# Kernel tuning notes

Measured on AMD Instinct MI355X. Metric: run time of the kernel, lower is better.

The kernel has to match this reference:

```python
import jax, jax.numpy as jnp
import numpy as np

B, S, H, D = 2, 2048, 16, 64
HID = H * D
NEG_INF = -10000.0

def setup_inputs() -> dict:
    key = jax.random.key(0)
    ks = jax.random.split(key, 4)
    std = 0.02
    return {
        'x': jax.random.normal(ks[0], (B, S, HID), dtype=jnp.float32),
        'mask': jnp.ones((B, S), dtype=jnp.int32),
        'Wq': jax.random.normal(ks[1], (HID, HID), dtype=jnp.float32) * std,
        'bq': jnp.zeros((HID,), dtype=jnp.float32),
        'Wk': jax.random.normal(ks[2], (HID, HID), dtype=jnp.float32) * std,
        'bk': jnp.zeros((HID,), dtype=jnp.float32),
        'Wv': jax.random.normal(ks[3], (HID, HID), dtype=jnp.float32) * std,
        'bv': jnp.zeros((HID,), dtype=jnp.float32),
    }

def reference(x, mask, Wq, bq, Wk, bk, Wv, bv):
    b, s, _ = x.shape
    def split_heads(t):  # [b,s,HID] -> [b,H,s,D]
        return t.reshape(b, s, H, D).transpose(0, 2, 1, 3)
    q = split_heads(x @ Wq + bq)
    k = split_heads(x @ Wk + bk)
    v = split_heads(x @ Wv + bv)
    scores = jnp.einsum('bhqd,bhkd->bhqk', q, k) / jnp.sqrt(jnp.float32(D))
    # additive padding mask: [b,1,1,s] broadcast over query positions and heads
    adder = (1.0 - mask.astype(scores.dtype))[:, None, None, :] * NEG_INF
    probs = jax.nn.softmax(scores + adder, axis=-1)
    ctx = jnp.einsum('bhqk,bhkd->bhqd', probs, v)  # [b,H,s,D]
    return ctx.transpose(0, 2, 1, 3).reshape(b, s, HID)
```

## Files before the change

### kernel.cpp

```cpp
#include <hip/hip_runtime.h>
#include <cstddef>

constexpr int Bc = 2, Sc = 2048, Hc = 16, Dc = 64, HIDc = 1024;
#define NEG_INF -10000.0f
#define LOG2E 1.44269504088896340736f

typedef _Float16 half8  __attribute__((ext_vector_type(8)));
typedef _Float16 half4  __attribute__((ext_vector_type(4)));
typedef float   floatx4 __attribute__((ext_vector_type(4)));

__device__ __forceinline__ void gload_lds16(const void* g, void* l) {
    __builtin_amdgcn_global_load_lds(
        (const __attribute__((address_space(1))) unsigned int*)g,
        (__attribute__((address_space(3))) unsigned int*)l, 16, 0, 0);
}

__global__ __launch_bounds__(256) void cvt_x_kernel(const float* __restrict__ x,
                                                    _Float16* __restrict__ xh) {
    int i = (blockIdx.x * 256 + threadIdx.x) * 8;
    float4 a = *(const float4*)(x + i);
    float4 b = *(const float4*)(x + i + 4);
    half8 h;
    h[0] = (_Float16)a.x; h[1] = (_Float16)a.y; h[2] = (_Float16)a.z; h[3] = (_Float16)a.w;
    h[4] = (_Float16)b.x; h[5] = (_Float16)b.y; h[6] = (_Float16)b.z; h[7] = (_Float16)b.w;
    *(half8*)(xh + i) = h;
}

__global__ __launch_bounds__(256) void cvt_w_kernel(const float* __restrict__ Wq,
                                                    const float* __restrict__ Wk,
                                                    const float* __restrict__ Wv,
                                                    _Float16* __restrict__ Wt) {
    const float* W = (blockIdx.z == 0) ? Wq : (blockIdx.z == 1) ? Wk : Wv;
    _Float16* out = Wt + (size_t)blockIdx.z * HIDc * HIDc;
    __shared__ _Float16 T[64][65];
    const int t = threadIdx.x;
    const int kb = blockIdx.x * 64, nb = blockIdx.y * 64;
    const int r = t >> 2, c4 = (t & 3) * 16;
    #pragma unroll
    for (int i = 0; i < 16; i += 4) {
        float4 a = *(const float4*)(W + (size_t)(kb + r) * HIDc + nb + c4 + i);
        T[c4 + i + 0][r] = (_Float16)a.x;
        T[c4 + i + 1][r] = (_Float16)a.y;
        T[c4 + i + 2][r] = (_Float16)a.z;
        T[c4 + i + 3][r] = (_Float16)a.w;
    }
    __syncthreads();
    const int n = t >> 2, k4 = (t & 3) * 16;
    half8 o0, o1;
    #pragma unroll
    for (int j = 0; j < 8; ++j) { o0[j] = T[n][k4 + j]; o1[j] = T[n][k4 + 8 + j]; }
    *(half8*)(out + (size_t)(nb + n) * HIDc + kb + k4)     = o0;
    *(half8*)(out + (size_t)(nb + n) * HIDc + kb + k4 + 8) = o1;
}

__global__ __launch_bounds__(256, 3) void proj_kernel(
    const _Float16* __restrict__ xh, const _Float16* __restrict__ Wt,
    const float* __restrict__ bq, const float* __restrict__ bk, const float* __restrict__ bv,
    _Float16* __restrict__ qw, _Float16* __restrict__ kw, _Float16* __restrict__ vt)
{
    const int z = blockIdx.z;
    const _Float16* Wz = Wt + (size_t)z * HIDc * HIDc;
    const float* bias = (z == 0) ? bq : (z == 1) ? bk : bv;

    __shared__ __align__(16) _Float16 SM[2][2][128 * 32];

    const int t = threadIdx.x;
    const int lane = t & 63, w = t >> 6;
    const int quad = lane >> 4, l16 = lane & 15;
    const int m0 = blockIdx.y * 128, n0 = blockIdx.x * 128;
    const int wm = (w >> 1) * 64, wn = (w & 1) * 64;

    const int srl = lane >> 2;
    const int ssl = (lane & 3) ^ ((lane >> 3) & 3);

    floatx4 acc[4][4];
    #pragma unroll
    for (int mb = 0; mb < 4; ++mb)
        #pragma unroll
        for (int nb = 0; nb < 4; ++nb) acc[mb][nb] = floatx4{0.f, 0.f, 0.f, 0.f};

    auto stage = [&](int buf, int kt) {
        #pragma unroll
        for (int j = 0; j < 2; ++j) {
            const int rb = (w + 4 * j) * 16;
            gload_lds16(xh + (size_t)(m0 + rb + srl) * HIDc + kt + ssl * 8,
                        &SM[buf][0][rb * 32]);
            gload_lds16(Wz + (size_t)(n0 + rb + srl) * HIDc + kt + ssl * 8,
                        &SM[buf][1][rb * 32]);
        }
    };

    stage(0, 0);
    __syncthreads();

    const int sA = (quad ^ ((l16 >> 1) & 3)) * 8;

    #pragma unroll 2
    for (int it = 0; it < HIDc / 32; ++it) {
        const int cur = it & 1;
        const int kn = (it + 1 < HIDc / 32) ? (it + 1) * 32 : 0;
        stage(cur ^ 1, kn);

        half8 af[4], bf[4];
        #pragma unroll
        for (int mb = 0; mb < 4; ++mb)
            af[mb] = *(const half8*)(&SM[cur][0][(wm + mb * 16 + l16) * 32 + sA]);
        #pragma unroll
        for (int nb = 0; nb < 4; ++nb)
            bf[nb] = *(const half8*)(&SM[cur][1][(wn + nb * 16 + l16) * 32 + sA]);
        #pragma unroll
        for (int mb = 0; mb < 4; ++mb)
            #pragma unroll
            for (int nb = 0; nb < 4; ++nb)
                acc[mb][nb] = __builtin_amdgcn_mfma_f32_16x16x32_f16(
                    af[mb], bf[nb], acc[mb][nb], 0, 0, 0);
        __syncthreads();
    }

    if (z == 2) {
        _Float16* T = (_Float16*)SM;
        const int bI0 = m0 >> 11, m0s = m0 & (Sc - 1);
        #pragma unroll
        for (int p = 0; p < 2; ++p) {
            __syncthreads();
            if ((w & 1) == p) {
                #pragma unroll
                for (int nb = 0; nb < 4; ++nb) {
                    const int n = nb * 16 + l16;
                    const float bi = bias[n0 + p * 64 + n];
                    #pragma unroll
                    for (int mb = 0; mb < 4; ++mb) {
                        half4 h4;
                        #pragma unroll
                        for (int r = 0; r < 4; ++r)
                            h4[r] = (_Float16)(acc[mb][nb][r] + bi);
                        *(half4*)(T + n * 136 + wm + mb * 16 + quad * 4) = h4;
                    }
                }
            }
            __syncthreads();
            const int n = t >> 2;
            const int N = n0 + p * 64 + n, hh = N >> 6, d = N & 63;
            _Float16* vrow = vt + (((size_t)(bI0 * Hc + hh)) * Dc + d) * Sc + m0s;
            #pragma unroll
            for (int j = 0; j < 4; ++j) {
                const int c = (t & 3) * 32 + j * 8;
                *(uint4*)(vrow + c) = *(const uint4*)(T + n * 136 + c);
            }
        }
        return;
    }
    #pragma unroll
    for (int nb = 0; nb < 4; ++nb) {
        const int N = n0 + wn + nb * 16 + l16;
        const float bi = bias[N];
        const int h = N >> 6, d = N & 63;
        #pragma unroll
        for (int mb = 0; mb < 4; ++mb) {
            #pragma unroll
            for (int r = 0; r < 4; ++r) {
                const int M = m0 + wm + mb * 16 + quad * 4 + r;
                const int bI = M >> 11, s = M & (Sc - 1);
                const float v = acc[mb][nb][r] + bi;
                if (z == 0)
                    qw[(((size_t)(bI * Hc + h)) * Sc + s) * Dc + d] =
                        (_Float16)(v * (0.125f * LOG2E));
                else
                    kw[(((size_t)(bI * Hc + h)) * Sc + s) * Dc + d] = (_Float16)v;
            }
        }
    }
}

__global__ __launch_bounds__(256, 2) void attn_kernel(
    const _Float16* __restrict__ qw, const _Float16* __restrict__ kw,
    const _Float16* __restrict__ vt, const int* __restrict__ mask,
    float* __restrict__ out)
{
    __shared__ __align__(16) float adder[Sc];
    __shared__ __align__(16) _Float16 Ks[2][64][72];
    __shared__ __align__(16) _Float16 Vs[2][64][72];

    const int t = threadIdx.x;
    const int lane = t & 63, w = t >> 6;
    const int quad = lane >> 4, l16 = lane & 15;
    const int bh = blockIdx.y;
    const int bI = bh >> 4, h = bh & 15;

    const _Float16* Qp = qw + (size_t)bh * Sc * Dc;
    const _Float16* Kp = kw + (size_t)bh * Sc * Dc;
    const _Float16* Vp = vt + (size_t)bh * Dc * Sc;

    const int srow = t >> 3;
    const int scol = (t & 7) * 8;
    const int m7 = t & 7;
    const int vc0 = 32 * (m7 & 1) + 4 * (m7 >> 1);

    {
        const int4* mp = (const int4*)(mask + bI * Sc);
        #pragma unroll
        for (int i = 0; i < 2; ++i) {
            int4 m4 = mp[t * 2 + i];
            int base = (t * 2 + i) * 4;
            adder[base + 0] = (1.0f - (float)m4.x) * (NEG_INF * LOG2E);
            adder[base + 1] = (1.0f - (float)m4.y) * (NEG_INF * LOG2E);
            adder[base + 2] = (1.0f - (float)m4.z) * (NEG_INF * LOG2E);
            adder[base + 3] = (1.0f - (float)m4.w) * (NEG_INF * LOG2E);
        }
    }
    #pragma unroll
    for (int hf = 0; hf < 2; ++hf) {
        const int row = srow + 32 * hf;
        uint4 kv = *(const uint4*)(Kp + (size_t)row * Dc + scol);
        uint4 vv = *(const uint4*)(Vp + (size_t)row * Sc + scol);
        *(uint4*)(&Ks[0][row][scol]) = kv;
        *(uint2*)(&Vs[0][row][vc0])      = make_uint2(vv.x, vv.y);
        *(uint2*)(&Vs[0][row][vc0 + 16]) = make_uint2(vv.z, vv.w);
    }

    const int qrow = blockIdx.x * 128 + w * 32;
    half8 aq[2][2];
    #pragma unroll
    for (int s = 0; s < 2; ++s)
        #pragma unroll
        for (int hh = 0; hh < 2; ++hh)
            aq[s][hh] = *(const half8*)(Qp + (size_t)(qrow + 16 * s + l16) * Dc
                                        + hh * 32 + quad * 8);

    floatx4 o[2][4], osum[2];
    #pragma unroll
    for (int s = 0; s < 2; ++s) {
        osum[s] = floatx4{0.f, 0.f, 0.f, 0.f};
        #pragma unroll
        for (int db = 0; db < 4; ++db) o[s][db] = floatx4{0.f, 0.f, 0.f, 0.f};
    }
    const half4 ones4 = {(_Float16)1.f, (_Float16)1.f, (_Float16)1.f, (_Float16)1.f};

    __syncthreads();

    #pragma unroll 2
    for (int it = 0; it < Sc / 64; ++it) {
        const int cur = it & 1;
        const int kt = it * 64;
        const int ktn = (it + 1 < Sc / 64) ? kt + 64 : 0;
        uint4 kstg[2], vstg[2];
        #pragma unroll
        for (int hf = 0; hf < 2; ++hf) {
            const int row = srow + 32 * hf;
            kstg[hf] = *(const uint4*)(Kp + (size_t)(ktn + row) * Dc + scol);
            vstg[hf] = *(const uint4*)(Vp + (size_t)row * Sc + ktn + scol);
        }

        half8 kb[4][2];
        #pragma unroll
        for (int nb = 0; nb < 4; ++nb)
            #pragma unroll
            for (int hh = 0; hh < 2; ++hh)
                kb[nb][hh] = *(const half8*)(&Ks[cur][nb * 16 + l16][hh * 32 + quad * 8]);

        half4 vb[4][4];
        #pragma unroll
        for (int db = 0; db < 4; ++db)
            #pragma unroll
            for (int hf2 = 0; hf2 < 2; ++hf2) {
                const half8 v8 = *(const half8*)(&Vs[cur][db * 16 + l16][quad * 16 + hf2 * 8]);
                vb[hf2 * 2 + 0][db] = __builtin_shufflevector(v8, v8, 0, 1, 2, 3);
                vb[hf2 * 2 + 1][db] = __builtin_shufflevector(v8, v8, 4, 5, 6, 7);
            }

        floatx4 st[2][4];
        __builtin_amdgcn_s_setprio(1);
        #pragma unroll
        for (int nb = 0; nb < 4; ++nb) {
            const floatx4 adv = *(const floatx4*)(&adder[kt + nb * 16 + quad * 4]);
            #pragma unroll
            for (int s = 0; s < 2; ++s) {
                floatx4 x0 = __builtin_amdgcn_mfma_f32_16x16x32_f16(kb[nb][0], aq[s][0], adv, 0, 0, 0);
                st[s][nb]  = __builtin_amdgcn_mfma_f32_16x16x32_f16(kb[nb][1], aq[s][1], x0, 0, 0, 0);
            }
        }
        __builtin_amdgcn_s_setprio(0);

        half4 pa[2][4];
        #pragma unroll
        for (int s = 0; s < 2; ++s)
            #pragma unroll
            for (int nb = 0; nb < 4; ++nb)
                #pragma unroll
                for (int r = 0; r < 4; ++r)
                    pa[s][nb][r] = (_Float16)__builtin_amdgcn_exp2f(st[s][nb][r]);

        __builtin_amdgcn_s_setprio(1);
        #pragma unroll
        for (int s = 0; s < 2; ++s)
            #pragma unroll
            for (int nb = 0; nb < 4; ++nb) {
                osum[s] = __builtin_amdgcn_mfma_f32_16x16x16f16(pa[s][nb], ones4, osum[s], 0, 0, 0);
                #pragma unroll
                for (int db = 0; db < 4; ++db)
                    o[s][db] = __builtin_amdgcn_mfma_f32_16x16x16f16(
                        pa[s][nb], vb[nb][db], o[s][db], 0, 0, 0);
            }
        __builtin_amdgcn_s_setprio(0);

        #pragma unroll
        for (int hf = 0; hf < 2; ++hf) {
            const int row = srow + 32 * hf;
            *(uint4*)(&Ks[cur ^ 1][row][scol]) = kstg[hf];
            const uint4 vv = vstg[hf];
            *(uint2*)(&Vs[cur ^ 1][row][vc0])      = make_uint2(vv.x, vv.y);
            *(uint2*)(&Vs[cur ^ 1][row][vc0 + 16]) = make_uint2(vv.z, vv.w);
        }
        __syncthreads();
    }

    float* op = out + (size_t)bI * Sc * HIDc + h * Dc;
    #pragma unroll
    for (int s = 0; s < 2; ++s)
        #pragma unroll
        for (int r = 0; r < 4; ++r) {
            const float inv = __builtin_amdgcn_rcpf(osum[s][r]);
            const int q = qrow + 16 * s + quad * 4 + r;
            #pragma unroll
            for (int db = 0; db < 4; ++db)
                op[(size_t)q * HIDc + db * 16 + l16] = o[s][db][r] * inv;
        }
}

extern "C" void kernel_launch(void* const* d_in, const int* in_sizes, int n_in,
                              void* d_out, int out_size, void* d_ws, size_t ws_size,
                              hipStream_t stream) {
    const float* x    = (const float*)d_in[0];
    const int*   mask = (const int*)  d_in[1];
    const float* Wq   = (const float*)d_in[2];
    const float* bq   = (const float*)d_in[3];
    const float* Wk   = (const float*)d_in[4];
    const float* bk   = (const float*)d_in[5];
    const float* Wv   = (const float*)d_in[6];
    const float* bv   = (const float*)d_in[7];
    float* out = (float*)d_out;

    char* ws = (char*)d_ws;
    _Float16* xh = (_Float16*)(ws);
    _Float16* Wt = (_Float16*)(ws + (size_t)8  * 1024 * 1024);
    _Float16* qw = (_Float16*)(ws + (size_t)14 * 1024 * 1024);
    _Float16* kw = (_Float16*)(ws + (size_t)22 * 1024 * 1024);
    _Float16* vt = (_Float16*)(ws + (size_t)30 * 1024 * 1024);

    cvt_x_kernel<<<(Bc * Sc * HIDc) / (256 * 8), 256, 0, stream>>>(x, xh);
    cvt_w_kernel<<<dim3(HIDc / 64, HIDc / 64, 3), 256, 0, stream>>>(Wq, Wk, Wv, Wt);
    proj_kernel<<<dim3(HIDc / 128, (Bc * Sc) / 128, 3), 256, 0, stream>>>(
        xh, Wt, bq, bk, bv, qw, kw, vt);
    attn_kernel<<<dim3(Sc / 128, Bc * Hc), 256, 0, stream>>>(qw, kw, vt, mask, out);
}
```

Measured before the change: 168.5 us.

## Load V fragments directly from global and stage 128-key K tiles in LDS

V is no longer staged through shared memory. Each wave reads its V MFMA operands straight from global memory (the transposed V layout) as half4 loads. K tiles grow from 64 to 128 keys per iteration, and each iteration processes two 64-key halves, which halves the number of barriers and LDS double-buffer swaps. The cost is redundant per-wave global loads of V that rely on cache hits, plus direct global-load latency that sits in front of the PV MFMAs with no prefetch.

```diff
diff --git a/kernel.cpp b/kernel.cpp
--- a/kernel.cpp
+++ b/kernel.cpp
@@ -178,8 +178,7 @@
     float* __restrict__ out)
 {
     __shared__ __align__(16) float adder[Sc];
-    __shared__ __align__(16) _Float16 Ks[2][64][72];
-    __shared__ __align__(16) _Float16 Vs[2][64][72];
+    __shared__ __align__(16) _Float16 Ks[2][128][72];
 
     const int t = threadIdx.x;
     const int lane = t & 63, w = t >> 6;
@@ -191,10 +190,8 @@
     const _Float16* Kp = kw + (size_t)bh * Sc * Dc;
     const _Float16* Vp = vt + (size_t)bh * Dc * Sc;
 
-    const int srow = t >> 3;
-    const int scol = (t & 7) * 8;
-    const int m7 = t & 7;
-    const int vc0 = 32 * (m7 & 1) + 4 * (m7 >> 1);
+    const int srow = t >> 1;
+    const int scol = (t & 1) * 32;
 
     {
         const int4* mp = (const int4*)(mask + bI * Sc);
@@ -208,14 +205,11 @@
             adder[base + 3] = (1.0f - (float)m4.w) * (NEG_INF * LOG2E);
         }
     }
-    #pragma unroll
-    for (int hf = 0; hf < 2; ++hf) {
-        const int row = srow + 32 * hf;
-        uint4 kv = *(const uint4*)(Kp + (size_t)row * Dc + scol);
-        uint4 vv = *(const uint4*)(Vp + (size_t)row * Sc + scol);
-        *(uint4*)(&Ks[0][row][scol]) = kv;
-        *(uint2*)(&Vs[0][row][vc0])      = make_uint2(vv.x, vv.y);
-        *(uint2*)(&Vs[0][row][vc0 + 16]) = make_uint2(vv.z, vv.w);
+    {
+        const _Float16* kp = Kp + (size_t)srow * Dc + scol;
+        #pragma unroll
+        for (int j = 0; j < 4; ++j)
+            *(uint4*)(&Ks[0][srow][scol + j * 8]) = *(const uint4*)(kp + j * 8);
     }
 
     const int qrow = blockIdx.x * 128 + w * 32;
@@ -239,78 +233,76 @@
     __syncthreads();
 
     #pragma unroll 2
-    for (int it = 0; it < Sc / 64; ++it) {
+    for (int it = 0; it < Sc / 128; ++it) {
         const int cur = it & 1;
-        const int kt = it * 64;
-        const int ktn = (it + 1 < Sc / 64) ? kt + 64 : 0;
-        uint4 kstg[2], vstg[2];
-        #pragma unroll
-        for (int hf = 0; hf < 2; ++hf) {
-            const int row = srow + 32 * hf;
-            kstg[hf] = *(const uint4*)(Kp + (size_t)(ktn + row) * Dc + scol);
-            vstg[hf] = *(const uint4*)(Vp + (size_t)row * Sc + ktn + scol);
-        }
-
-        half8 kb[4][2];
-        #pragma unroll
-        for (int nb = 0; nb < 4; ++nb)
-            #pragma unroll
-            for (int hh = 0; hh < 2; ++hh)
-                kb[nb][hh] = *(const half8*)(&Ks[cur][nb * 16 + l16][hh * 32 + quad * 8]);
-
-        half4 vb[4][4];
-        #pragma unroll
-        for (int db = 0; db < 4; ++db)
-            #pragma unroll
-            for (int hf2 = 0; hf2 < 2; ++hf2) {
-                const half8 v8 = *(const half8*)(&Vs[cur][db * 16 + l16][quad * 16 + hf2 * 8]);
-                vb[hf2 * 2 + 0][db] = __builtin_shufflevector(v8, v8, 0, 1, 2, 3);
-                vb[hf2 * 2 + 1][db] = __builtin_shufflevector(v8, v8, 4, 5, 6, 7);
+        const int kt = it * 128;
+        const int ktn = (it + 1 < Sc / 128) ? kt + 128 : 0;
+        uint4 ks[4];
+        {
+            const _Float16* kp = Kp + (size_t)(ktn + srow) * Dc + scol;
+            #pragma unroll
+            for (int j = 0; j < 4; ++j) ks[j] = *(const uint4*)(kp + j * 8);
+        }
+
+        #pragma unroll
+        for (int hb = 0; hb < 2; ++hb) {
+            const int kb0 = hb * 64;
+
+            half4 vb[4][4];
+            #pragma unroll
+            for (int nb = 0; nb < 4; ++nb)
+                #pragma unroll
+                for (int db = 0; db < 4; ++db)
+                    vb[nb][db] = *(const half4*)(
+                        Vp + (size_t)(db * 16 + l16) * Sc + kt + kb0 + nb * 16 + quad * 4);
+
+            half8 kb[4][2];
+            #pragma unroll
+            for (int nb = 0; nb < 4; ++nb)
+                #pragma unroll
+                for (int hh = 0; hh < 2; ++hh)
+                    kb[nb][hh] = *(const half8*)(
+                        &Ks[cur][kb0 + nb * 16 + l16][hh * 32 + quad * 8]);
+
+            floatx4 st[2][4];
+            __builtin_amdgcn_s_setprio(1);
+            #pragma unroll
+            for (int nb = 0; nb < 4; ++nb) {
+                const floatx4 adv = *(const floatx4*)(&adder[kt + kb0 + nb * 16 + quad * 4]);
+                #pragma unroll
+                for (int s = 0; s < 2; ++s) {
+                    floatx4 x0 = __builtin_amdgcn_mfma_f32_16x16x32_f16(kb[nb][0], aq[s][0], adv, 0, 0, 0);
+                    st[s][nb]  = __builtin_amdgcn_mfma_f32_16x16x32_f16(kb[nb][1], aq[s][1], x0, 0, 0, 0);
+                }
             }
-
-        floatx4 st[2][4];
-        __builtin_amdgcn_s_setprio(1);
-        #pragma unroll
-        for (int nb = 0; nb < 4; ++nb) {
-            const floatx4 adv = *(const floatx4*)(&adder[kt + nb * 16 + quad * 4]);
-            #pragma unroll
-            for (int s = 0; s < 2; ++s) {
-                floatx4 x0 = __builtin_amdgcn_mfma_f32_16x16x32_f16(kb[nb][0], aq[s][0], adv, 0, 0, 0);
-                st[s][nb]  = __builtin_amdgcn_mfma_f32_16x16x32_f16(kb[nb][1], aq[s][1], x0, 0, 0, 0);
-            }
-        }
-        __builtin_amdgcn_s_setprio(0);
-
-        half4 pa[2][4];
-        #pragma unroll
-        for (int s = 0; s < 2; ++s)
-            #pragma unroll
-            for (int nb = 0; nb < 4; ++nb)
-                #pragma unroll
-                for (int r = 0; r < 4; ++r)
-                    pa[s][nb][r] = (_Float16)__builtin_amdgcn_exp2f(st[s][nb][r]);
-
-        __builtin_amdgcn_s_setprio(1);
-        #pragma unroll
-        for (int s = 0; s < 2; ++s)
-            #pragma unroll
-            for (int nb = 0; nb < 4; ++nb) {
-                osum[s] = __builtin_amdgcn_mfma_f32_16x16x16f16(pa[s][nb], ones4, osum[s], 0, 0, 0);
-                #pragma unroll
-                for (int db = 0; db < 4; ++db)
-                    o[s][db] = __builtin_amdgcn_mfma_f32_16x16x16f16(
-                        pa[s][nb], vb[nb][db], o[s][db], 0, 0, 0);
-            }
-        __builtin_amdgcn_s_setprio(0);
-
-        #pragma unroll
-        for (int hf = 0; hf < 2; ++hf) {
-            const int row = srow + 32 * hf;
-            *(uint4*)(&Ks[cur ^ 1][row][scol]) = kstg[hf];
-            const uint4 vv = vstg[hf];
-            *(uint2*)(&Vs[cur ^ 1][row][vc0])      = make_uint2(vv.x, vv.y);
-            *(uint2*)(&Vs[cur ^ 1][row][vc0 + 16]) = make_uint2(vv.z, vv.w);
-        }
+            __builtin_amdgcn_s_setprio(0);
+
+            half4 pa[2][4];
+            #pragma unroll
+            for (int s = 0; s < 2; ++s)
+                #pragma unroll
+                for (int nb = 0; nb < 4; ++nb)
+                    #pragma unroll
+                    for (int r = 0; r < 4; ++r)
+                        pa[s][nb][r] = (_Float16)__builtin_amdgcn_exp2f(st[s][nb][r]);
+
+            __builtin_amdgcn_s_setprio(1);
+            #pragma unroll
+            for (int s = 0; s < 2; ++s)
+                #pragma unroll
+                for (int nb = 0; nb < 4; ++nb) {
+                    osum[s] = __builtin_amdgcn_mfma_f32_16x16x16f16(pa[s][nb], ones4, osum[s], 0, 0, 0);
+                    #pragma unroll
+                    for (int db = 0; db < 4; ++db)
+                        o[s][db] = __builtin_amdgcn_mfma_f32_16x16x16f16(
+                            pa[s][nb], vb[nb][db], o[s][db], 0, 0, 0);
+                }
+            __builtin_amdgcn_s_setprio(0);
+        }
+
+        #pragma unroll
+        for (int j = 0; j < 4; ++j)
+            *(uint4*)(&Ks[cur ^ 1][srow][scol + j * 8]) = ks[j];
         __syncthreads();
     }
 
```

Measured after the change: 244.5 us. 45.1% more time.
